# Optimization experiments

Hardware: AMD Instinct MI355X
Metric: run time of the kernel (lower is better)

The kernel has to match this reference:

```python
import jax, jax.numpy as jnp
import numpy as np

B, H, S, D = 2, 16, 2048, 64  # depth = dmodel / num_heads
DMODEL = H * D


def setup_inputs() -> dict:
    key = jax.random.key(0)
    kq, kk, kv, kw = jax.random.split(key, 4)
    Q = jax.random.normal(kq, (B, H, S, D), dtype=jnp.float32)
    K = jax.random.normal(kk, (B, H, S, D), dtype=jnp.float32)
    V = jax.random.normal(kv, (B, H, S, D), dtype=jnp.float32)
    W = jax.random.normal(kw, (DMODEL, DMODEL), dtype=jnp.float32) * (1.0 / np.sqrt(DMODEL))
    b = jnp.zeros((DMODEL,), dtype=jnp.float32)
    return {"Q": Q, "K": K, "V": V, "W": W, "b": b}


def reference(Q, K, V, W, b):
    depth = Q.shape[-1]
    # scores: (B, H, S, S) -- full score matrix, matching the original math
    scores = jnp.einsum('bhqd,bhkd->bhqk', Q, K) / jnp.sqrt(jnp.float32(depth))
    attn = jax.nn.softmax(scores, axis=-1)
    vals = jnp.einsum('bhqk,bhkd->bhqd', attn, V)          # (B, H, S, D)
    vals = jnp.transpose(vals, (0, 2, 1, 3))               # (B, S, H, D)
    concat = vals.reshape(vals.shape[0], vals.shape[1], -1)  # (B, S, dmodel)
    return concat @ W + b
```

## Files before the change

### kernel.cpp

```cpp
#include <hip/hip_runtime.h>
#include <hip/hip_bf16.h>


typedef float  f32x16 __attribute__((ext_vector_type(16)));
typedef float  f32x4v __attribute__((ext_vector_type(4)));
typedef float  f32x2v __attribute__((ext_vector_type(2)));
typedef __bf16 bf16x8 __attribute__((ext_vector_type(8)));
typedef __bf16 bf16x4 __attribute__((ext_vector_type(4)));
typedef __bf16 bf16x2 __attribute__((ext_vector_type(2)));

static constexpr int Bn = 2, Hn = 16, Sn = 2048, Dn = 64, DM = 1024;
static constexpr size_t QKV_ELEMS = (size_t)Bn * Hn * Sn * Dn;

#define QSCALE 0.18033688011112042f

#define LGKM_BARRIER() do {                                  \
    asm volatile("s_waitcnt lgkmcnt(0)" ::: "memory");       \
    __builtin_amdgcn_s_barrier();                            \
  } while (0)

#if __has_builtin(__builtin_amdgcn_cvt_pk_bf16_f32)
static __device__ __forceinline__ unsigned pack2(float a, float b) {
  bf16x2 t = __builtin_amdgcn_cvt_pk_bf16_f32(a, b);
  union { bf16x2 v; unsigned u; } c; c.v = t; return c.u;
}
#else
static __device__ __forceinline__ unsigned pack2(float a, float b) {
  union { __bf16 h; unsigned short s; } ua, ub;
  ua.h = (__bf16)a; ub.h = (__bf16)b;
  return (unsigned)ua.s | ((unsigned)ub.s << 16);
}
#endif

static __device__ __forceinline__ void unzip8(const unsigned* wds, bf16x8* r0, bf16x8* r1) {
  union { unsigned u[4]; bf16x8 v; } a, b;
#pragma unroll
  for (int i = 0; i < 4; ++i) {
    unsigned lo = wds[2 * i], hi = wds[2 * i + 1];
    a.u[i] = (lo & 0xffffu) | (hi << 16);
    b.u[i] = (lo >> 16) | (hi & 0xffff0000u);
  }
  *r0 = a.v; *r1 = b.v;
}

__global__ __launch_bounds__(256) void convert_all(
    const float* __restrict__ k,
    const float* __restrict__ v, const float* __restrict__ w,
    __bf16* __restrict__ ko,
    __bf16* __restrict__ vt, __bf16* __restrict__ wt) {
  __shared__ __bf16 T[64][74];
  const int bid = blockIdx.x, t = threadIdx.x;

  if (bid < 2048) {
    size_t i = ((size_t)bid * 256 + t) * 8;
    f32x4v a = *(const f32x4v*)(k + i);
    f32x4v b = *(const f32x4v*)(k + i + 4);
    bf16x8 o;
#pragma unroll
    for (int j = 0; j < 4; ++j) { o[j] = (__bf16)a[j]; o[4 + j] = (__bf16)b[j]; }
    *(bf16x8*)(ko + i) = o;
    return;
  }

  const float* s0;
  __bf16* dst0;
  size_t dst_stride;
  {
    const int r = t >> 2, c0 = (t & 3) * 16;
    if (bid < 3072) {
      const int idx = bid - 2048;
      const int kv0 = (idx & 31) * 64, bh = idx >> 5;
      s0 = v + ((size_t)bh * Sn + kv0 + r) * Dn + c0;
      dst0 = vt + (size_t)bh * Dn * Sn + kv0;
      dst_stride = Sn;
    } else {
      const int idx = bid - 3072;
      const int nt = (idx & 15) * 64, kt = (idx >> 4) * 64;
      s0 = w + (size_t)(kt + r) * DM + nt + c0;
      dst0 = wt + (size_t)nt * DM + kt;
      dst_stride = DM;
    }
    union { bf16x8 v8; unsigned u[4]; } o0, o1;
#pragma unroll
    for (int i = 0; i < 2; ++i) {
      f32x4v f = *(const f32x4v*)(s0 + i * 4);
#pragma unroll
      for (int j = 0; j < 4; ++j) o0.v8[i * 4 + j] = (__bf16)f[j];
    }
#pragma unroll
    for (int i = 0; i < 2; ++i) {
      f32x4v f = *(const f32x4v*)(s0 + 8 + i * 4);
#pragma unroll
      for (int j = 0; j < 4; ++j) o1.v8[i * 4 + j] = (__bf16)f[j];
    }
#pragma unroll
    for (int j = 0; j < 4; ++j) {
      *(unsigned*)&T[r][c0 + 2 * j]     = o0.u[j];
      *(unsigned*)&T[r][c0 + 8 + 2 * j] = o1.u[j];
    }
  }
  __syncthreads();
  const int rp = t >> 3, k0 = (t & 7) * 8;
  unsigned wds[8];
#pragma unroll
  for (int i = 0; i < 8; ++i) wds[i] = *(const unsigned*)&T[k0 + i][2 * rp];
  bf16x8 r0, r1; unzip8(wds, &r0, &r1);
  __bf16* d0 = dst0 + (size_t)(2 * rp) * dst_stride + k0;
  *(bf16x8*)d0 = r0;
  *(bf16x8*)(d0 + dst_stride) = r1;
}

__global__ __launch_bounds__(512, 4) void attn(
    const float* __restrict__ Qf, const __bf16* __restrict__ Kb,
    const __bf16* __restrict__ Vtg, __bf16* __restrict__ Cc) {
  const int tid = threadIdx.x;
  const int wave = tid >> 6, lane = tid & 63;
  const int ln = lane & 31, g = lane >> 5;
  const int qg = wave >> 1, kh = wave & 1;
  const int f = blockIdx.x;
  const int swz = (f & 7) * 64 + (f >> 3);
  const int qb = swz & 15, h = (swz >> 4) & 15, bz = swz >> 8;

  __shared__ __bf16 Ks[2][128][72];
  __shared__ __bf16 Vs[2][64][136];

  const size_t hoff = (size_t)(bz * Hn + h) * Sn * Dn;
  const float*  Qp = Qf + hoff + (size_t)(qb * 128 + qg * 32) * Dn;
  const __bf16* Kp = Kb + hoff;
  const __bf16* Vp = Vtg + hoff;

  bf16x8 qf[4];
#pragma unroll
  for (int ks = 0; ks < 4; ++ks) {
    const float* qp = Qp + (size_t)ln * Dn + ks * 16 + g * 8;
    f32x4v f0 = *(const f32x4v*)qp;
    f32x4v f1 = *(const f32x4v*)(qp + 4);
#pragma unroll
    for (int j = 0; j < 4; ++j) {
      qf[ks][j]     = (__bf16)(f0[j] * QSCALE);
      qf[ks][4 + j] = (__bf16)(f1[j] * QSCALE);
    }
  }

  const int kr = tid >> 2, kc = (tid & 3) * 16;
  const int vr = tid >> 3, vc = (tid & 7) * 16;
  const __bf16* kbase = Kp + (size_t)kr * Dn + kc;
  const __bf16* vbase = Vp + (size_t)vr * Sn + vc;

  bf16x8 k0r = *(const bf16x8*)kbase, k1r = *(const bf16x8*)(kbase + 8);
  bf16x8 v0r = *(const bf16x8*)vbase, v1r = *(const bf16x8*)(vbase + 8);
  {
    *(bf16x8*)&Ks[0][kr][kc]     = k0r;
    *(bf16x8*)&Ks[0][kr][kc + 8] = k1r;
    union { bf16x8 v; bf16x4 h[2]; } u0, u1; u0.v = v0r; u1.v = v1r;
    union { bf16x4 h[2]; bf16x8 v; } w0, w1;
    w0.h[0] = u0.h[0]; w0.h[1] = u1.h[0];
    w1.h[0] = u0.h[1]; w1.h[1] = u1.h[1];
    *(bf16x8*)&Vs[0][vr][vc]     = w0.v;
    *(bf16x8*)&Vs[0][vr][vc + 8] = w1.v;
  }
  k0r = *(const bf16x8*)(kbase + (size_t)128 * Dn);
  k1r = *(const bf16x8*)(kbase + (size_t)128 * Dn + 8);
  v0r = *(const bf16x8*)(vbase + 128);
  v1r = *(const bf16x8*)(vbase + 128 + 8);
  LGKM_BARRIER();

  f32x16 O0 = {}, O1 = {};
  float Lown = 0.0f;
  constexpr int NT = Sn / 128;

  for (int kt = 0; kt < NT; ++kt) {
    const int buf = kt & 1;

    unsigned w[16];
#pragma unroll
    for (int m = 0; m < 2; ++m) {
      bf16x8 kf[4];
#pragma unroll
      for (int ks = 0; ks < 4; ++ks)
        kf[ks] = *(const bf16x8*)&Ks[buf][kh * 64 + m * 32 + ln][ks * 16 + g * 8];

      f32x16 s = {};
      __builtin_amdgcn_s_setprio(1);
#pragma unroll
      for (int ks = 0; ks < 4; ++ks)
        s = __builtin_amdgcn_mfma_f32_32x32x16_bf16(kf[ks], qf[ks], s, 0, 0, 0);
      __builtin_amdgcn_s_setprio(0);

      float p[16];
#pragma unroll
      for (int r = 0; r < 16; ++r) p[r] = __builtin_amdgcn_exp2f(s[r]);
      f32x2v s2 = {0.0f, 0.0f};
#pragma unroll
      for (int tt = 0; tt < 8; ++tt) { f32x2v t2 = {p[2 * tt], p[2 * tt + 1]}; s2 += t2; }
      Lown += s2[0] + s2[1];
#pragma unroll
      for (int tt = 0; tt < 8; ++tt) w[m * 8 + tt] = pack2(p[2 * tt], p[2 * tt + 1]);
    }

    if (kt + 1 < NT) {
      const int nb = buf ^ 1;
      *(bf16x8*)&Ks[nb][kr][kc]     = k0r;
      *(bf16x8*)&Ks[nb][kr][kc + 8] = k1r;
      union { bf16x8 v; bf16x4 h[2]; } u0, u1; u0.v = v0r; u1.v = v1r;
      union { bf16x4 h[2]; bf16x8 v; } w0, w1;
      w0.h[0] = u0.h[0]; w0.h[1] = u1.h[0];
      w1.h[0] = u0.h[1]; w1.h[1] = u1.h[1];
      *(bf16x8*)&Vs[nb][vr][vc]     = w0.v;
      *(bf16x8*)&Vs[nb][vr][vc + 8] = w1.v;
      if (kt + 2 < NT) {
        const __bf16* kp = kbase + (size_t)(kt + 2) * 128 * Dn;
        k0r = *(const bf16x8*)kp; k1r = *(const bf16x8*)(kp + 8);
        const __bf16* vp = vbase + (kt + 2) * 128;
        v0r = *(const bf16x8*)vp; v1r = *(const bf16x8*)(vp + 8);
      }
    }

    __builtin_amdgcn_s_setprio(1);
#pragma unroll
    for (int s4 = 0; s4 < 4; ++s4) {
      const int cb = kh * 64 + s4 * 16 + g * 8;
      bf16x8 vf0 = *(const bf16x8*)&Vs[buf][ln][cb];
      bf16x8 vf1 = *(const bf16x8*)&Vs[buf][32 + ln][cb];
      union { unsigned u[4]; bf16x8 v; } pu;
      pu.u[0] = w[s4 * 4 + 0];
      pu.u[1] = w[s4 * 4 + 1];
      pu.u[2] = w[s4 * 4 + 2];
      pu.u[3] = w[s4 * 4 + 3];
      O0 = __builtin_amdgcn_mfma_f32_32x32x16_bf16(vf0, pu.v, O0, 0, 0, 0);
      O1 = __builtin_amdgcn_mfma_f32_32x32x16_bf16(vf1, pu.v, O1, 0, 0, 0);
    }
    __builtin_amdgcn_s_setprio(0);

    LGKM_BARRIER();
  }

  const float Lred = Lown + __shfl_xor(Lown, 32);
  float* Ex = (float*)Ks;
  const int slot = (qg * 64 + lane) * 36;
  if (kh == 1) {
#pragma unroll
    for (int i = 0; i < 4; ++i) {
      f32x4v t = {O0[4 * i], O0[4 * i + 1], O0[4 * i + 2], O0[4 * i + 3]};
      *(f32x4v*)&Ex[slot + 4 * i] = t;
    }
#pragma unroll
    for (int i = 0; i < 4; ++i) {
      f32x4v t = {O1[4 * i], O1[4 * i + 1], O1[4 * i + 2], O1[4 * i + 3]};
      *(f32x4v*)&Ex[slot + 16 + 4 * i] = t;
    }
    Ex[slot + 32] = Lred;
  }
  __syncthreads();
  __bf16* T = (__bf16*)Vs;
  if (kh == 0) {
    float inv;
#pragma unroll
    for (int i = 0; i < 4; ++i) {
      f32x4v t = *(const f32x4v*)&Ex[slot + 4 * i];
#pragma unroll
      for (int c = 0; c < 4; ++c) O0[4 * i + c] += t[c];
    }
#pragma unroll
    for (int i = 0; i < 4; ++i) {
      f32x4v t = *(const f32x4v*)&Ex[slot + 16 + 4 * i];
#pragma unroll
      for (int c = 0; c < 4; ++c) O1[4 * i + c] += t[c];
    }
    inv = 1.0f / (Lred + Ex[slot + 32]);
#pragma unroll
    for (int dh = 0; dh < 2; ++dh) {
#pragma unroll
      for (int a = 0; a < 4; ++a) {
        const f32x16 O = dh ? O1 : O0;
        bf16x4 t4;
#pragma unroll
        for (int c = 0; c < 4; ++c) t4[c] = (__bf16)(O[4 * a + c] * inv);
        *(bf16x4*)&T[(qg * 32 + ln) * 72 + dh * 32 + 8 * a + 4 * g] = t4;
      }
    }
  }
  __syncthreads();
  const int q0 = qb * 128;
#pragma unroll
  for (int i = 0; i < 2; ++i) {
    const int rq = i * 64 + (tid >> 3);
    const int c8 = (tid & 7) * 8;
    bf16x8 o = *(const bf16x8*)&T[rq * 72 + c8];
    size_t base = (((size_t)bz * Sn + q0 + rq) * Hn + h) * Dn + c8;
    *(bf16x8*)&Cc[base] = o;
  }
}

__global__ __launch_bounds__(512, 2) void proj(
    const __bf16* __restrict__ A, const __bf16* __restrict__ Wt,
    const float* __restrict__ bias, float* __restrict__ out) {
  const int tid = threadIdx.x, wave = tid >> 6, lane = tid & 63;
  const int ln = lane & 31, g = lane >> 5;
  const int mq = wave >> 1, nh = wave & 1;
  const int f = blockIdx.x;
  const int idx = f >> 3;
  const int bn = idx & 15;
  const int bm = (f & 7) * 4 + (idx >> 4);
  __shared__ __bf16 As[2][128][72];
  __shared__ __bf16 Bs[2][64][72];
  const int ar = tid >> 2, ac = (tid & 3) * 16;
  const int rb = tid >> 3, cb = (tid & 7) * 8;
  f32x16 acc = {};
  const __bf16* Ap = A + (size_t)(bm * 128) * DM;
  const __bf16* Wp = Wt + (size_t)(bn * 64) * DM;

  bf16x8 a0, a1, b0;
  {
    const __bf16* ap = Ap + (size_t)ar * DM + ac;
    a0 = *(const bf16x8*)ap; a1 = *(const bf16x8*)(ap + 8);
    b0 = *(const bf16x8*)(Wp + (size_t)rb * DM + cb);
  }
  *(bf16x8*)&As[0][ar][ac]     = a0;
  *(bf16x8*)&As[0][ar][ac + 8] = a1;
  *(bf16x8*)&Bs[0][rb][cb]     = b0;
  {
    const __bf16* ap = Ap + (size_t)ar * DM + 64 + ac;
    a0 = *(const bf16x8*)ap; a1 = *(const bf16x8*)(ap + 8);
    b0 = *(const bf16x8*)(Wp + (size_t)rb * DM + 64 + cb);
  }
  LGKM_BARRIER();

  constexpr int KT = DM / 64;
  for (int kt = 0; kt < KT; ++kt) {
    const int buf = kt & 1;
    __builtin_amdgcn_s_setprio(1);
#pragma unroll
    for (int ks = 0; ks < 4; ++ks) {
      bf16x8 af = *(const bf16x8*)&As[buf][mq * 32 + ln][ks * 16 + g * 8];
      bf16x8 wf = *(const bf16x8*)&Bs[buf][nh * 32 + ln][ks * 16 + g * 8];
      acc = __builtin_amdgcn_mfma_f32_32x32x16_bf16(af, wf, acc, 0, 0, 0);
    }
    __builtin_amdgcn_s_setprio(0);
    if (kt + 1 < KT) {
      const int nb = buf ^ 1;
      *(bf16x8*)&As[nb][ar][ac]     = a0;
      *(bf16x8*)&As[nb][ar][ac + 8] = a1;
      *(bf16x8*)&Bs[nb][rb][cb]     = b0;
      if (kt + 2 < KT) {
        const __bf16* ap = Ap + (size_t)ar * DM + (kt + 2) * 64 + ac;
        a0 = *(const bf16x8*)ap; a1 = *(const bf16x8*)(ap + 8);
        b0 = *(const bf16x8*)(Wp + (size_t)rb * DM + (kt + 2) * 64 + cb);
      }
    }
    LGKM_BARRIER();
  }
  const float bv = bias[bn * 64 + nh * 32 + ln];
#pragma unroll
  for (int r = 0; r < 16; ++r) {
    int row = bm * 128 + mq * 32 + (r & 3) + 8 * (r >> 2) + 4 * g;
    out[(size_t)row * DM + bn * 64 + nh * 32 + ln] = acc[r] + bv;
  }
}

extern "C" void kernel_launch(void* const* d_in, const int* in_sizes, int n_in,
                              void* d_out, int out_size, void* d_ws, size_t ws_size,
                              hipStream_t stream) {
  const float* Q = (const float*)d_in[0];
  const float* K = (const float*)d_in[1];
  const float* V = (const float*)d_in[2];
  const float* W = (const float*)d_in[3];
  const float* b = (const float*)d_in[4];
  float* out = (float*)d_out;

  __bf16* ws  = (__bf16*)d_ws;
  __bf16* Kb  = ws;
  __bf16* Vtg = Kb + QKV_ELEMS;
  __bf16* Cc  = Vtg + QKV_ELEMS;
  __bf16* Wt  = Cc + QKV_ELEMS;

  convert_all<<<dim3(3328, 1, 1), 256, 0, stream>>>(K, V, W, Kb, Vtg, Wt);
  attn<<<dim3(512, 1, 1), 512, 0, stream>>>(Q, Kb, Vtg, Cc);
  proj<<<dim3(512, 1, 1), 512, 0, stream>>>(Cc, Wt, b, out);
}
```

Measured before the change: 153.2 us.

## Drop LDS staging in attention and projection, load MFMA operands from global

Removes the double-buffered shared-memory staging of K/V tiles in the attention kernel and of A/W tiles in the projection kernel. Each wave now loads its MFMA operands directly from global memory, relying on L1/L2 caching, and the per-tile barriers go away. The aim is to cut LDS traffic, barrier stalls and LDS footprint, and the projection kernel's occupancy hint is raised. The cost is redundant global loads across waves that share K/V rows, plus fragmented 8-byte V loads and no explicit prefetch, so more load latency is exposed.

```diff
diff --git a/kernel.cpp b/kernel.cpp
--- a/kernel.cpp
+++ b/kernel.cpp
@@ -13,11 +13,6 @@
 static constexpr size_t QKV_ELEMS = (size_t)Bn * Hn * Sn * Dn;
 
 #define QSCALE 0.18033688011112042f
-
-#define LGKM_BARRIER() do {                                  \
-    asm volatile("s_waitcnt lgkmcnt(0)" ::: "memory");       \
-    __builtin_amdgcn_s_barrier();                            \
-  } while (0)
 
 #if __has_builtin(__builtin_amdgcn_cvt_pk_bf16_f32)
 static __device__ __forceinline__ unsigned pack2(float a, float b) {
@@ -113,6 +108,9 @@
 __global__ __launch_bounds__(512, 4) void attn(
     const float* __restrict__ Qf, const __bf16* __restrict__ Kb,
     const __bf16* __restrict__ Vtg, __bf16* __restrict__ Cc) {
+  __shared__ float  Ex[256 * 36];
+  __shared__ __bf16 T[128][72];
+
   const int tid = threadIdx.x;
   const int wave = tid >> 6, lane = tid & 63;
   const int ln = lane & 31, g = lane >> 5;
@@ -121,9 +119,6 @@
   const int swz = (f & 7) * 64 + (f >> 3);
   const int qb = swz & 15, h = (swz >> 4) & 15, bz = swz >> 8;
 
-  __shared__ __bf16 Ks[2][128][72];
-  __shared__ __bf16 Vs[2][64][136];
-
   const size_t hoff = (size_t)(bz * Hn + h) * Sn * Dn;
   const float*  Qp = Qf + hoff + (size_t)(qb * 128 + qg * 32) * Dn;
   const __bf16* Kp = Kb + hoff;
@@ -142,50 +137,24 @@
     }
   }
 
-  const int kr = tid >> 2, kc = (tid & 3) * 16;
-  const int vr = tid >> 3, vc = (tid & 7) * 16;
-  const __bf16* kbase = Kp + (size_t)kr * Dn + kc;
-  const __bf16* vbase = Vp + (size_t)vr * Sn + vc;
-
-  bf16x8 k0r = *(const bf16x8*)kbase, k1r = *(const bf16x8*)(kbase + 8);
-  bf16x8 v0r = *(const bf16x8*)vbase, v1r = *(const bf16x8*)(vbase + 8);
-  {
-    *(bf16x8*)&Ks[0][kr][kc]     = k0r;
-    *(bf16x8*)&Ks[0][kr][kc + 8] = k1r;
-    union { bf16x8 v; bf16x4 h[2]; } u0, u1; u0.v = v0r; u1.v = v1r;
-    union { bf16x4 h[2]; bf16x8 v; } w0, w1;
-    w0.h[0] = u0.h[0]; w0.h[1] = u1.h[0];
-    w1.h[0] = u0.h[1]; w1.h[1] = u1.h[1];
-    *(bf16x8*)&Vs[0][vr][vc]     = w0.v;
-    *(bf16x8*)&Vs[0][vr][vc + 8] = w1.v;
-  }
-  k0r = *(const bf16x8*)(kbase + (size_t)128 * Dn);
-  k1r = *(const bf16x8*)(kbase + (size_t)128 * Dn + 8);
-  v0r = *(const bf16x8*)(vbase + 128);
-  v1r = *(const bf16x8*)(vbase + 128 + 8);
-  LGKM_BARRIER();
-
   f32x16 O0 = {}, O1 = {};
   float Lown = 0.0f;
   constexpr int NT = Sn / 128;
 
   for (int kt = 0; kt < NT; ++kt) {
-    const int buf = kt & 1;
-
     unsigned w[16];
 #pragma unroll
     for (int m = 0; m < 2; ++m) {
+      const __bf16* krow = Kp + (size_t)(kt * 128 + kh * 64 + m * 32 + ln) * Dn;
       bf16x8 kf[4];
 #pragma unroll
       for (int ks = 0; ks < 4; ++ks)
-        kf[ks] = *(const bf16x8*)&Ks[buf][kh * 64 + m * 32 + ln][ks * 16 + g * 8];
+        kf[ks] = *(const bf16x8*)(krow + ks * 16 + g * 8);
 
       f32x16 s = {};
-      __builtin_amdgcn_s_setprio(1);
 #pragma unroll
       for (int ks = 0; ks < 4; ++ks)
         s = __builtin_amdgcn_mfma_f32_32x32x16_bf16(kf[ks], qf[ks], s, 0, 0, 0);
-      __builtin_amdgcn_s_setprio(0);
 
       float p[16];
 #pragma unroll
@@ -198,45 +167,27 @@
       for (int tt = 0; tt < 8; ++tt) w[m * 8 + tt] = pack2(p[2 * tt], p[2 * tt + 1]);
     }
 
-    if (kt + 1 < NT) {
-      const int nb = buf ^ 1;
-      *(bf16x8*)&Ks[nb][kr][kc]     = k0r;
-      *(bf16x8*)&Ks[nb][kr][kc + 8] = k1r;
-      union { bf16x8 v; bf16x4 h[2]; } u0, u1; u0.v = v0r; u1.v = v1r;
-      union { bf16x4 h[2]; bf16x8 v; } w0, w1;
-      w0.h[0] = u0.h[0]; w0.h[1] = u1.h[0];
-      w1.h[0] = u0.h[1]; w1.h[1] = u1.h[1];
-      *(bf16x8*)&Vs[nb][vr][vc]     = w0.v;
-      *(bf16x8*)&Vs[nb][vr][vc + 8] = w1.v;
-      if (kt + 2 < NT) {
-        const __bf16* kp = kbase + (size_t)(kt + 2) * 128 * Dn;
-        k0r = *(const bf16x8*)kp; k1r = *(const bf16x8*)(kp + 8);
-        const __bf16* vp = vbase + (kt + 2) * 128;
-        v0r = *(const bf16x8*)vp; v1r = *(const bf16x8*)(vp + 8);
-      }
-    }
-
-    __builtin_amdgcn_s_setprio(1);
 #pragma unroll
     for (int s4 = 0; s4 < 4; ++s4) {
-      const int cb = kh * 64 + s4 * 16 + g * 8;
-      bf16x8 vf0 = *(const bf16x8*)&Vs[buf][ln][cb];
-      bf16x8 vf1 = *(const bf16x8*)&Vs[buf][32 + ln][cb];
+      const int base16 = kt * 128 + kh * 64 + s4 * 16 + g * 4;
+      const __bf16* v0p = Vp + (size_t)ln * Sn + base16;
+      const __bf16* v1p = Vp + (size_t)(32 + ln) * Sn + base16;
+      union { bf16x4 h[2]; bf16x8 v; } u0, u1;
+      u0.h[0] = *(const bf16x4*)(v0p);
+      u0.h[1] = *(const bf16x4*)(v0p + 8);
+      u1.h[0] = *(const bf16x4*)(v1p);
+      u1.h[1] = *(const bf16x4*)(v1p + 8);
       union { unsigned u[4]; bf16x8 v; } pu;
       pu.u[0] = w[s4 * 4 + 0];
       pu.u[1] = w[s4 * 4 + 1];
       pu.u[2] = w[s4 * 4 + 2];
       pu.u[3] = w[s4 * 4 + 3];
-      O0 = __builtin_amdgcn_mfma_f32_32x32x16_bf16(vf0, pu.v, O0, 0, 0, 0);
-      O1 = __builtin_amdgcn_mfma_f32_32x32x16_bf16(vf1, pu.v, O1, 0, 0, 0);
-    }
-    __builtin_amdgcn_s_setprio(0);
-
-    LGKM_BARRIER();
+      O0 = __builtin_amdgcn_mfma_f32_32x32x16_bf16(u0.v, pu.v, O0, 0, 0, 0);
+      O1 = __builtin_amdgcn_mfma_f32_32x32x16_bf16(u1.v, pu.v, O1, 0, 0, 0);
+    }
   }
 
   const float Lred = Lown + __shfl_xor(Lown, 32);
-  float* Ex = (float*)Ks;
   const int slot = (qg * 64 + lane) * 36;
   if (kh == 1) {
 #pragma unroll
@@ -252,7 +203,6 @@
     Ex[slot + 32] = Lred;
   }
   __syncthreads();
-  __bf16* T = (__bf16*)Vs;
   if (kh == 0) {
     float inv;
 #pragma unroll
@@ -276,7 +226,7 @@
         bf16x4 t4;
 #pragma unroll
         for (int c = 0; c < 4; ++c) t4[c] = (__bf16)(O[4 * a + c] * inv);
-        *(bf16x4*)&T[(qg * 32 + ln) * 72 + dh * 32 + 8 * a + 4 * g] = t4;
+        *(bf16x4*)&T[qg * 32 + ln][dh * 32 + 8 * a + 4 * g] = t4;
       }
     }
   }
@@ -286,13 +236,13 @@
   for (int i = 0; i < 2; ++i) {
     const int rq = i * 64 + (tid >> 3);
     const int c8 = (tid & 7) * 8;
-    bf16x8 o = *(const bf16x8*)&T[rq * 72 + c8];
+    bf16x8 o = *(const bf16x8*)&T[rq][c8];
     size_t base = (((size_t)bz * Sn + q0 + rq) * Hn + h) * Dn + c8;
     *(bf16x8*)&Cc[base] = o;
   }
 }
 
-__global__ __launch_bounds__(512, 2) void proj(
+__global__ __launch_bounds__(512, 4) void proj(
     const __bf16* __restrict__ A, const __bf16* __restrict__ Wt,
     const float* __restrict__ bias, float* __restrict__ out) {
   const int tid = threadIdx.x, wave = tid >> 6, lane = tid & 63;
@@ -302,53 +252,19 @@
   const int idx = f >> 3;
   const int bn = idx & 15;
   const int bm = (f & 7) * 4 + (idx >> 4);
-  __shared__ __bf16 As[2][128][72];
-  __shared__ __bf16 Bs[2][64][72];
-  const int ar = tid >> 2, ac = (tid & 3) * 16;
-  const int rb = tid >> 3, cb = (tid & 7) * 8;
+
+  const __bf16* aRow = A  + (size_t)(bm * 128 + mq * 32 + ln) * DM;
+  const __bf16* wRow = Wt + (size_t)(bn * 64 + nh * 32 + ln) * DM;
   f32x16 acc = {};
-  const __bf16* Ap = A + (size_t)(bm * 128) * DM;
-  const __bf16* Wp = Wt + (size_t)(bn * 64) * DM;
-
-  bf16x8 a0, a1, b0;
-  {
-    const __bf16* ap = Ap + (size_t)ar * DM + ac;
-    a0 = *(const bf16x8*)ap; a1 = *(const bf16x8*)(ap + 8);
-    b0 = *(const bf16x8*)(Wp + (size_t)rb * DM + cb);
-  }
-  *(bf16x8*)&As[0][ar][ac]     = a0;
-  *(bf16x8*)&As[0][ar][ac + 8] = a1;
-  *(bf16x8*)&Bs[0][rb][cb]     = b0;
-  {
-    const __bf16* ap = Ap + (size_t)ar * DM + 64 + ac;
-    a0 = *(const bf16x8*)ap; a1 = *(const bf16x8*)(ap + 8);
-    b0 = *(const bf16x8*)(Wp + (size_t)rb * DM + 64 + cb);
-  }
-  LGKM_BARRIER();
-
-  constexpr int KT = DM / 64;
-  for (int kt = 0; kt < KT; ++kt) {
-    const int buf = kt & 1;
-    __builtin_amdgcn_s_setprio(1);
+#pragma unroll 4
+  for (int kt = 0; kt < 16; ++kt) {
 #pragma unroll
     for (int ks = 0; ks < 4; ++ks) {
-      bf16x8 af = *(const bf16x8*)&As[buf][mq * 32 + ln][ks * 16 + g * 8];
-      bf16x8 wf = *(const bf16x8*)&Bs[buf][nh * 32 + ln][ks * 16 + g * 8];
+      const int ko = kt * 64 + ks * 16 + g * 8;
+      bf16x8 af = *(const bf16x8*)(aRow + ko);
+      bf16x8 wf = *(const bf16x8*)(wRow + ko);
       acc = __builtin_amdgcn_mfma_f32_32x32x16_bf16(af, wf, acc, 0, 0, 0);
     }
-    __builtin_amdgcn_s_setprio(0);
-    if (kt + 1 < KT) {
-      const int nb = buf ^ 1;
-      *(bf16x8*)&As[nb][ar][ac]     = a0;
-      *(bf16x8*)&As[nb][ar][ac + 8] = a1;
-      *(bf16x8*)&Bs[nb][rb][cb]     = b0;
-      if (kt + 2 < KT) {
-        const __bf16* ap = Ap + (size_t)ar * DM + (kt + 2) * 64 + ac;
-        a0 = *(const bf16x8*)ap; a1 = *(const bf16x8*)(ap + 8);
-        b0 = *(const bf16x8*)(Wp + (size_t)rb * DM + (kt + 2) * 64 + cb);
-      }
-    }
-    LGKM_BARRIER();
   }
   const float bv = bias[bn * 64 + nh * 32 + ln];
 #pragma unroll
```

New measurement: 329.5 us. 115% more time.

## Store attention output and weights in MFMA-fragment layout; drop LDS staging in proj

Applied to the files above, without the earlier changes.

The attention kernel and the weight-transpose prep kernel now write their bf16 outputs in a tiled layout of 32-row by 8-column fragments, each 256 elements, so every lane's MFMA operand is one contiguous 16-byte load. The projection GEMM then reads A and W fragments straight from global memory, with no LDS double buffering and no barriers, and its occupancy bound rises to 4 blocks. This removes LDS traffic and synchronisation from the projection. In exchange it relies on L2/L1 caching to reuse data across waves, since each wave now loads its own operands.

```diff
diff --git a/kernel.cpp b/kernel.cpp
--- a/kernel.cpp
+++ b/kernel.cpp
@@ -63,11 +63,13 @@
   }
 
   const float* s0;
-  __bf16* dst0;
-  size_t dst_stride;
+  __bf16* dst0 = nullptr;
+  size_t dst_stride = 0;
+  int nt_ = 0, kt_ = 0;
+  const bool isW = (bid >= 3072);
   {
     const int r = t >> 2, c0 = (t & 3) * 16;
-    if (bid < 3072) {
+    if (!isW) {
       const int idx = bid - 2048;
       const int kv0 = (idx & 31) * 64, bh = idx >> 5;
       s0 = v + ((size_t)bh * Sn + kv0 + r) * Dn + c0;
@@ -75,10 +77,8 @@
       dst_stride = Sn;
     } else {
       const int idx = bid - 3072;
-      const int nt = (idx & 15) * 64, kt = (idx >> 4) * 64;
-      s0 = w + (size_t)(kt + r) * DM + nt + c0;
-      dst0 = wt + (size_t)nt * DM + kt;
-      dst_stride = DM;
+      nt_ = (idx & 15) * 64; kt_ = (idx >> 4) * 64;
+      s0 = w + (size_t)(kt_ + r) * DM + nt_ + c0;
     }
     union { bf16x8 v8; unsigned u[4]; } o0, o1;
 #pragma unroll
@@ -105,9 +105,17 @@
 #pragma unroll
   for (int i = 0; i < 8; ++i) wds[i] = *(const unsigned*)&T[k0 + i][2 * rp];
   bf16x8 r0, r1; unzip8(wds, &r0, &r1);
-  __bf16* d0 = dst0 + (size_t)(2 * rp) * dst_stride + k0;
-  *(bf16x8*)d0 = r0;
-  *(bf16x8*)(d0 + dst_stride) = r1;
+  if (!isW) {
+    __bf16* d0 = dst0 + (size_t)(2 * rp) * dst_stride + k0;
+    *(bf16x8*)d0 = r0;
+    *(bf16x8*)(d0 + dst_stride) = r1;
+  } else {
+    const int n0 = nt_ + 2 * rp;
+    __bf16* d0 = wt + ((size_t)(n0 >> 5) * 128 + (kt_ >> 3) + (t & 7)) * 256
+                    + (n0 & 31) * 8;
+    *(bf16x8*)d0 = r0;
+    *(bf16x8*)(d0 + 8) = r1;
+  }
 }
 
 __global__ __launch_bounds__(512, 4) void attn(
@@ -287,13 +295,15 @@
     const int rq = i * 64 + (tid >> 3);
     const int c8 = (tid & 7) * 8;
     bf16x8 o = *(const bf16x8*)&T[rq * 72 + c8];
-    size_t base = (((size_t)bz * Sn + q0 + rq) * Hn + h) * Dn + c8;
+    const int m = bz * Sn + q0 + rq;
+    const int kg = h * 8 + (tid & 7);
+    size_t base = ((size_t)(m >> 5) * 128 + kg) * 256 + (m & 31) * 8;
     *(bf16x8*)&Cc[base] = o;
   }
 }
 
-__global__ __launch_bounds__(512, 2) void proj(
-    const __bf16* __restrict__ A, const __bf16* __restrict__ Wt,
+__global__ __launch_bounds__(512, 4) void proj(
+    const __bf16* __restrict__ A2, const __bf16* __restrict__ Wt2,
     const float* __restrict__ bias, float* __restrict__ out) {
   const int tid = threadIdx.x, wave = tid >> 6, lane = tid & 63;
   const int ln = lane & 31, g = lane >> 5;
@@ -302,53 +312,22 @@
   const int idx = f >> 3;
   const int bn = idx & 15;
   const int bm = (f & 7) * 4 + (idx >> 4);
-  __shared__ __bf16 As[2][128][72];
-  __shared__ __bf16 Bs[2][64][72];
-  const int ar = tid >> 2, ac = (tid & 3) * 16;
-  const int rb = tid >> 3, cb = (tid & 7) * 8;
+
+  const int mg = bm * 4 + mq;
+  const int ng = bn * 2 + nh;
+  const __bf16* Ab = A2  + (size_t)mg * 128 * 256 + (size_t)ln * 8;
+  const __bf16* Wb = Wt2 + (size_t)ng * 128 * 256 + (size_t)ln * 8;
+
   f32x16 acc = {};
-  const __bf16* Ap = A + (size_t)(bm * 128) * DM;
-  const __bf16* Wp = Wt + (size_t)(bn * 64) * DM;
-
-  bf16x8 a0, a1, b0;
-  {
-    const __bf16* ap = Ap + (size_t)ar * DM + ac;
-    a0 = *(const bf16x8*)ap; a1 = *(const bf16x8*)(ap + 8);
-    b0 = *(const bf16x8*)(Wp + (size_t)rb * DM + cb);
-  }
-  *(bf16x8*)&As[0][ar][ac]     = a0;
-  *(bf16x8*)&As[0][ar][ac + 8] = a1;
-  *(bf16x8*)&Bs[0][rb][cb]     = b0;
-  {
-    const __bf16* ap = Ap + (size_t)ar * DM + 64 + ac;
-    a0 = *(const bf16x8*)ap; a1 = *(const bf16x8*)(ap + 8);
-    b0 = *(const bf16x8*)(Wp + (size_t)rb * DM + 64 + cb);
-  }
-  LGKM_BARRIER();
-
-  constexpr int KT = DM / 64;
-  for (int kt = 0; kt < KT; ++kt) {
-    const int buf = kt & 1;
-    __builtin_amdgcn_s_setprio(1);
+#pragma unroll 4
+  for (int kt = 0; kt < 16; ++kt) {
 #pragma unroll
     for (int ks = 0; ks < 4; ++ks) {
-      bf16x8 af = *(const bf16x8*)&As[buf][mq * 32 + ln][ks * 16 + g * 8];
-      bf16x8 wf = *(const bf16x8*)&Bs[buf][nh * 32 + ln][ks * 16 + g * 8];
+      const size_t off = (size_t)(kt * 8 + ks * 2 + g) * 256;
+      bf16x8 af = *(const bf16x8*)(Ab + off);
+      bf16x8 wf = *(const bf16x8*)(Wb + off);
       acc = __builtin_amdgcn_mfma_f32_32x32x16_bf16(af, wf, acc, 0, 0, 0);
     }
-    __builtin_amdgcn_s_setprio(0);
-    if (kt + 1 < KT) {
-      const int nb = buf ^ 1;
-      *(bf16x8*)&As[nb][ar][ac]     = a0;
-      *(bf16x8*)&As[nb][ar][ac + 8] = a1;
-      *(bf16x8*)&Bs[nb][rb][cb]     = b0;
-      if (kt + 2 < KT) {
-        const __bf16* ap = Ap + (size_t)ar * DM + (kt + 2) * 64 + ac;
-        a0 = *(const bf16x8*)ap; a1 = *(const bf16x8*)(ap + 8);
-        b0 = *(const bf16x8*)(Wp + (size_t)rb * DM + (kt + 2) * 64 + cb);
-      }
-    }
-    LGKM_BARRIER();
   }
   const float bv = bias[bn * 64 + nh * 32 + ln];
 #pragma unroll
```

Result: slower. 159.4 us (+4.0%).
